# Performance work log

Measured on AMD Instinct MI355X. Metric: run time of the kernel, lower is better.

## Reference

```python
import jax, jax.numpy as jnp
import numpy as np
import math

B, S, H = 1, 2048, 2048
NH, NKV, HD = 32, 8, 64
GROUPS = NH // NKV
WINDOW = 128
ROPE_THETA = 150000.0
FACTOR = 32.0
ORIG_MAX = 4096.0
BETA_FAST = 32.0
BETA_SLOW = 1.0
SCALE = 1.0 / math.sqrt(HD)


def yarn_rope(q, k, position_ids):
    # q: [B,S,NH,HD], k: [B,S,NKV,HD]
    dim_half = HD // 2
    inv_freq = 1.0 / ROPE_THETA ** (jnp.arange(0, dim_half, 2, dtype=jnp.float32) / dim_half)
    wavelengths = 2.0 * jnp.pi / inv_freq
    ratio = ORIG_MAX / wavelengths
    alpha = jnp.clip((FACTOR * ratio - BETA_FAST) / (BETA_SLOW - BETA_FAST), 0.0, 1.0)
    inv_freq_scaled = inv_freq / FACTOR ** alpha
    freqs = position_ids[:, :, None].astype(jnp.float32) * inv_freq_scaled[None, None, :]
    freqs = jnp.repeat(freqs, 2, axis=-1)  # [B,S,dim_half]
    cos = jnp.cos(freqs)[:, :, None, :]
    sin = jnp.sin(freqs)[:, :, None, :]

    def rotate_half(x):
        # Faithful to source: x already has last dim == dim_half, so x2 is empty
        # and rotate_half(x) == x. Kept literal for exactness.
        x1 = x[..., :dim_half]
        x2 = x[..., dim_half:]
        return jnp.concatenate([-x2, x1], axis=-1)

    q_rot = q[..., :dim_half]
    k_rot = k[..., :dim_half]
    q_rot = q_rot * cos + rotate_half(q_rot) * sin
    k_rot = k_rot * cos + rotate_half(k_rot) * sin
    q = jnp.concatenate([q_rot, q[..., dim_half:]], axis=-1)
    k = jnp.concatenate([k_rot, k[..., dim_half:]], axis=-1)
    return q, k


def setup_inputs() -> dict:
    key = jax.random.key(0)
    ks = jax.random.split(key, 5)
    std = 0.02
    hidden_states = jax.random.normal(ks[0], (B, S, H), dtype=jnp.float32)
    position_ids = jnp.broadcast_to(jnp.arange(S, dtype=jnp.int32)[None, :], (B, S))
    Wq = jax.random.normal(ks[1], (H, NH * HD), dtype=jnp.float32) * std
    Wk = jax.random.normal(ks[2], (H, NKV * HD), dtype=jnp.float32) * std
    Wv = jax.random.normal(ks[3], (H, NKV * HD), dtype=jnp.float32) * std
    Wo = jax.random.normal(ks[4], (NH * HD, H), dtype=jnp.float32) * std
    return {"hidden_states": hidden_states, "position_ids": position_ids,
            "Wq": Wq, "Wk": Wk, "Wv": Wv, "Wo": Wo}


def reference(hidden_states, position_ids, Wq, Wk, Wv, Wo):
    q = (hidden_states @ Wq).reshape(B, S, NH, HD)
    k = (hidden_states @ Wk).reshape(B, S, NKV, HD)
    v = (hidden_states @ Wv).reshape(B, S, NKV, HD)
    q, k = yarn_rope(q, k, position_ids)
    # GQA: repeat kv heads to match query heads
    k = jnp.repeat(k, GROUPS, axis=2)  # [B,S,NH,HD]
    v = jnp.repeat(v, GROUPS, axis=2)
    # scores: [B,NH,S,S]
    scores = jnp.einsum('bqhd,bkhd->bhqk', q, k) * SCALE
    row = jnp.arange(S)[:, None]
    col = jnp.arange(S)[None, :]
    mask = ((jnp.abs(row - col) <= WINDOW) & (row >= col)).astype(jnp.float32)
    scores = scores + (1.0 - mask)[None, None, :, :] * -1e9
    attn = jax.nn.softmax(scores, axis=-1)
    out = jnp.einsum('bhqk,bkhd->bqhd', attn, v).reshape(B, S, NH * HD)
    return out @ Wo
```

## Files before the change

kernel.cpp:

```cpp
#include <hip/hip_runtime.h>

typedef unsigned short u16;
typedef short short8 __attribute__((ext_vector_type(8)));
typedef float f32x4 __attribute__((ext_vector_type(4)));

#define SLEN 2048
#define QKV_LD 3072
#define KOFF 2048
#define VOFF 2560

__device__ __forceinline__ u16 f2b(float f){
  unsigned u = __float_as_uint(f);
  u = u + 0x7FFFu + ((u >> 16) & 1u);
  return (u16)(u >> 16);
}
__device__ __forceinline__ float b2f(u16 v){
  unsigned u = ((unsigned)v) << 16;
  return __uint_as_float(u);
}

__device__ __forceinline__ void gload16(const u16* g, u16* l){
  __builtin_amdgcn_global_load_lds((const __attribute__((address_space(1))) void*)g,
                                   (__attribute__((address_space(3))) void*)l, 16, 0, 0);
}

__global__ __launch_bounds__(256) void k_prep(const float* __restrict__ hidden, u16* __restrict__ hb,
                                              const int* __restrict__ pos, float* __restrict__ g,
                                              const float* __restrict__ Wq, const float* __restrict__ Wk,
                                              const float* __restrict__ Wv,
                                              u16* __restrict__ Wcat){
  __shared__ float tile[64][68];
  int b = blockIdx.x, t = threadIdx.x;
  if (b < 4096){
    int i = b * 256 + t;
    float4 v = ((const float4*)hidden)[i];
    ushort4 o;
    o.x = f2b(v.x); o.y = f2b(v.y); o.z = f2b(v.z); o.w = f2b(v.w);
    ((ushort4*)hb)[i] = o;
    return;
  }
  if (b < 4224){
    int idx = (b - 4096) * 256 + t;
    int s = idx >> 4, i = idx & 15;
    float inv = 1.0f / powf(150000.0f, (float)i / 16.0f);
    float wl = 6.283185307179586f / inv;
    float ratio = 4096.0f / wl;
    float alpha = (32.0f * ratio - 32.0f) / (1.0f - 32.0f);
    alpha = fminf(fmaxf(alpha, 0.0f), 1.0f);
    float invs = inv / powf(32.0f, alpha);
    float th = (float)pos[s] * invs;
    double tt = (double)th;
    g[idx] = (float)(cos(tt) + sin(tt));
    return;
  }
  b -= 4224;
  const float* W; int Nw, rowoff;
  if (b < 1024)      { W = Wq; Nw = 2048; rowoff = 0; }
  else if (b < 1280) { W = Wk; Nw = 512;  rowoff = 2048; b -= 1024; }
  else               { W = Wv; Nw = 512;  rowoff = 2560; b -= 1280; }
  const int kt = b & 31, nt = b >> 5;
  const int k0 = kt * 64, n0 = nt * 64;
  #pragma unroll
  for (int i = 0; i < 4; ++i){
    int slot = i * 256 + t;
    int r = slot >> 4, c4 = (slot & 15) * 4;
    float4 v = *(const float4*)&W[(size_t)(k0 + r) * Nw + n0 + c4];
    tile[r][c4] = v.x; tile[r][c4+1] = v.y; tile[r][c4+2] = v.z; tile[r][c4+3] = v.w;
  }
  __syncthreads();
  #pragma unroll
  for (int i = 0; i < 4; ++i){
    int slot = i * 256 + t;
    int nl = slot >> 4, k4 = (slot & 15) * 4;
    ushort4 o;
    o.x = f2b(tile[k4][nl]);   o.y = f2b(tile[k4+1][nl]);
    o.z = f2b(tile[k4+2][nl]); o.w = f2b(tile[k4+3][nl]);
    *(ushort4*)&Wcat[(size_t)(rowoff + n0 + nl) * 2048 + k0 + k4] = o;
  }
}

template<int OUTF32, int ROPE, int BM, int BN, int MINW, int NBUF>
__global__ __launch_bounds__(256, MINW) void k_gemm(const u16* __restrict__ A, const u16* __restrict__ Bt,
                                                    void* __restrict__ C, const float* __restrict__ g,
                                                    int M, int N, int K){
  constexpr int AG = BM / 32;
  constexpr int BG = BN / 32;
  constexpr int ASZ = BM * 64;
  constexpr int BSZ = BN * 64;
  constexpr int MR = BM / 32;
  constexpr int NR = BN / 32;
  __shared__ __align__(16) u16 Smem[NBUF * (ASZ + BSZ)];
  const int tid = threadIdx.x;
  const int lane = tid & 63;
  const int w = tid >> 6;
  const int wr = (w >> 1) * (BM / 2);
  const int wc = (w & 1) * (BN / 2);

  const int nbx = M / BM;
  const int nb  = nbx * (N / BN);
  const int q8  = nb >> 3;
  const int bo  = blockIdx.x;
  const int id2 = (bo & 7) * q8 + (bo >> 3);
  const int m0 = (id2 % nbx) * BM;
  const int n0 = (id2 / nbx) * BN;

  const int rl = lane >> 3;
  const int sc = ((lane & 7) ^ rl) << 3;
  const u16* Ag[AG]; const u16* Bg[BG];
  int Ad[AG], Bd[BG];
  #pragma unroll
  for (int i = 0; i < AG; ++i){
    int row0 = w * (AG * 8) + i * 8;
    Ag[i] = A + (size_t)(m0 + row0 + rl) * K + sc;
    Ad[i] = row0 * 64;
  }
  #pragma unroll
  for (int i = 0; i < BG; ++i){
    int row0 = w * (BG * 8) + i * 8;
    Bg[i] = Bt + (size_t)(n0 + row0 + rl) * K + sc;
    Bd[i] = NBUF * ASZ + row0 * 64;
  }

  const int fr = lane & 15;
  const int g4 = lane >> 4;

  f32x4 acc[MR][NR] = {};

  auto stage = [&](int buf, int k0){
    #pragma unroll
    for (int i = 0; i < AG; ++i) gload16(Ag[i] + k0, Smem + Ad[i] + buf * ASZ);
    #pragma unroll
    for (int i = 0; i < BG; ++i) gload16(Bg[i] + k0, Smem + Bd[i] + buf * BSZ);
  };

  auto compute = [&](int buf){
    const u16* Asb = Smem + buf * ASZ;
    const u16* Bsb = Smem + NBUF * ASZ + buf * BSZ;
    #pragma unroll
    for (int kk = 0; kk < 2; ++kk){
      const int sw = (((kk * 4 + g4)) ^ (fr & 7)) << 3;
      short8 af[MR], bf[NR];
      #pragma unroll
      for (int m = 0; m < MR; ++m)
        af[m] = *(const short8*)&Asb[(wr + m * 16 + fr) * 64 + sw];
      #pragma unroll
      for (int j = 0; j < NR; ++j)
        bf[j] = *(const short8*)&Bsb[(wc + j * 16 + fr) * 64 + sw];
      #pragma unroll
      for (int m = 0; m < MR; ++m)
        #pragma unroll
        for (int j = 0; j < NR; ++j)
          acc[m][j] = __builtin_amdgcn_mfma_f32_16x16x32_bf16(af[m], bf[j], acc[m][j], 0, 0, 0);
    }
  };

  stage(0, 0);
  int buf = 0;
  const int nt = K >> 6;
  if constexpr (NBUF == 2){
    for (int kt = 0; kt < nt; ++kt){
      asm volatile("s_waitcnt vmcnt(0)" ::: "memory");
      __builtin_amdgcn_s_barrier();
      __builtin_amdgcn_sched_barrier(0);
      if (kt + 1 < nt) stage(buf ^ 1, (kt + 1) << 6);
      compute(buf);
      buf ^= 1;
    }
  } else {
    for (int kt = 0; kt < nt; ++kt){
      int nxt = (buf + 1 == NBUF) ? 0 : buf + 1;
      if (kt + 1 < nt){
        stage(nxt, (kt + 1) << 6);
        if constexpr (AG + BG == 6)      asm volatile("s_waitcnt vmcnt(6)" ::: "memory");
        else if constexpr (AG + BG == 7) asm volatile("s_waitcnt vmcnt(7)" ::: "memory");
        else                             asm volatile("s_waitcnt vmcnt(8)" ::: "memory");
      } else {
        asm volatile("s_waitcnt vmcnt(0)" ::: "memory");
      }
      __builtin_amdgcn_s_barrier();
      __builtin_amdgcn_sched_barrier(0);
      compute(buf);
      buf = nxt;
    }
  }

  const int r4 = g4 * 4;
  #pragma unroll
  for (int m = 0; m < MR; ++m)
    #pragma unroll
    for (int j = 0; j < NR; ++j)
      #pragma unroll
      for (int v = 0; v < 4; ++v){
        size_t row = (size_t)(m0 + wr + m * 16 + r4 + v);
        size_t col = (size_t)(n0 + wc + j * 16 + fr);
        float x = acc[m][j][v];
        if (OUTF32){
          ((float*)C)[row * N + col] = x;
        } else {
          if (ROPE){
            int c = (int)col;
            int cj = c & 63;
            if (c < 2560 && cj < 32) x *= g[row * 16 + (cj >> 1)];
            if (c < 2048) x *= 0.18033688f;
          }
          ((u16*)C)[row * N + col] = f2b(x);
        }
      }
}

#define PST 168
__global__ __launch_bounds__(512, 4) void k_attn(const u16* __restrict__ qkv, u16* __restrict__ aout,
                                                 const float* __restrict__ Wo, u16* __restrict__ Wot){
  __shared__ __align__(16) u16 Vt[64 * 264];
  __shared__ __align__(16) u16 P[8 * 16 * PST];
  const int tid = threadIdx.x;
  const int lane = tid & 63;
  const int w = tid >> 6;
  const int id = blockIdx.x;
  const int id2 = (id & 7) * 64 + (id >> 3);
  const int h = id2 >> 4;
  const int q0 = (id2 & 15) * 128;
  const int kvh = h >> 2;
  const int kv0 = q0 - 128;

  {
    const u16* Vg = qkv + VOFF + kvh * 64;
    #pragma unroll
    for (int i = 0; i < 4; ++i){
      int slot = i * 512 + tid;
      int kk = slot >> 3, d8 = (slot & 7) * 8;
      int ks = kv0 + kk; if (ks < 0) ks = 0;
      int ck = kk ^ ((d8 >> 4) << 3);
      short8 v = *(const short8*)(Vg + (size_t)ks * QKV_LD + d8);
      #pragma unroll
      for (int e = 0; e < 8; ++e) Vt[(d8 + e) * 264 + ck] = (u16)v[e];
    }
  }

  const int fr = lane & 15;
  const int kc8 = (lane >> 4) * 8;
  const int r4 = (lane >> 4) * 4;
  const int tt = w >> 2;
  const int wl = w & 3;
  const int nw0 = wl & ~1;
  const int c0 = nw0 * 16;
  const int qt = q0 + tt * 64;
  const int kbase = qt - 128;
  u16* Pw = P + w * 16 * PST;
  const u16* Qg = qkv + h * 64;
  const u16* Kg = qkv + KOFF + kvh * 64;

  short8 qa[2];
  {
    int qrow = qt + wl * 16 + fr;
    qa[0] = *(const short8*)(Qg + (size_t)qrow * QKV_LD + kc8);
    qa[1] = *(const short8*)(Qg + (size_t)qrow * QKV_LD + 32 + kc8);
  }

  f32x4 sc[10];
  __builtin_amdgcn_s_setprio(1);
  #pragma unroll
  for (int n = 0; n < 10; ++n){
    int kr = kbase + (nw0 + n) * 16 + fr;
    int krc = kr < 0 ? 0 : kr;
    short8 kb0 = *(const short8*)(Kg + (size_t)krc * QKV_LD + kc8);
    short8 kb1 = *(const short8*)(Kg + (size_t)krc * QKV_LD + 32 + kc8);
    f32x4 z = {0.f, 0.f, 0.f, 0.f};
    z = __builtin_amdgcn_mfma_f32_16x16x32_bf16(qa[0], kb0, z, 0, 0, 0);
    z = __builtin_amdgcn_mfma_f32_16x16x32_bf16(qa[1], kb1, z, 0, 0, 0);
    sc[n] = z;
  }
  __builtin_amdgcn_s_setprio(0);

  float inv_l[4];
  #pragma unroll
  for (int j = 0; j < 4; ++j){
    int q = qt + wl * 16 + r4 + j;
    float mx = -3.0e38f;
    #pragma unroll
    for (int n = 0; n < 10; ++n){
      int key = kbase + (nw0 + n) * 16 + fr;
      bool valid = (key >= 0) && (key <= q) && (key >= q - 128);
      float s = valid ? sc[n][j] : -1.0e30f;
      sc[n][j] = s;
      mx = fmaxf(mx, s);
    }
    mx = fmaxf(mx, __shfl_xor(mx, 1));
    mx = fmaxf(mx, __shfl_xor(mx, 2));
    mx = fmaxf(mx, __shfl_xor(mx, 4));
    mx = fmaxf(mx, __shfl_xor(mx, 8));
    float sum = 0.f;
    #pragma unroll
    for (int n = 0; n < 10; ++n){
      float pp = exp2f(sc[n][j] - mx);
      sc[n][j] = pp;
      sum += pp;
    }
    sum += __shfl_xor(sum, 1);
    sum += __shfl_xor(sum, 2);
    sum += __shfl_xor(sum, 4);
    sum += __shfl_xor(sum, 8);
    inv_l[j] = 1.0f / sum;
  }

  #pragma unroll
  for (int n = 0; n < 10; ++n)
    #pragma unroll
    for (int j = 0; j < 4; ++j)
      Pw[(r4 + j) * PST + n * 16 + fr] = f2b(sc[n][j]);

  asm volatile("s_waitcnt lgkmcnt(0)" ::: "memory");
  __syncthreads();

  f32x4 ov[4] = {};
  __builtin_amdgcn_s_setprio(1);
  #pragma unroll
  for (int kc = 0; kc < 5; ++kc){
    short8 pa = *(const short8*)&Pw[fr * PST + kc * 32 + kc8];
    #pragma unroll
    for (int f = 0; f < 4; ++f){
      short8 vb = *(const short8*)&Vt[(f * 16 + fr) * 264 + tt * 64 + c0 + kc * 32 + (kc8 ^ (f << 3))];
      ov[f] = __builtin_amdgcn_mfma_f32_16x16x32_bf16(pa, vb, ov[f], 0, 0, 0);
    }
  }
  __builtin_amdgcn_s_setprio(0);

  #pragma unroll
  for (int f = 0; f < 4; ++f)
    #pragma unroll
    for (int j = 0; j < 4; ++j){
      int q = qt + wl * 16 + r4 + j;
      int col = h * 64 + f * 16 + fr;
      aout[(size_t)q * 2048 + col] = f2b(ov[f][j] * inv_l[j]);
    }

  __syncthreads();
  float (*tf)[68] = (float(*)[68])Vt;
  #pragma unroll
  for (int tix = 0; tix < 2; ++tix){
    int tile = id * 2 + tix;
    int kt2 = tile & 31, nt2 = tile >> 5;
    int k0 = kt2 * 64, n0 = nt2 * 64;
    #pragma unroll
    for (int i = 0; i < 2; ++i){
      int slot = i * 512 + tid;
      int r = slot >> 4, c4 = (slot & 15) * 4;
      float4 v = *(const float4*)&Wo[(size_t)(k0 + r) * 2048 + n0 + c4];
      tf[r][c4] = v.x; tf[r][c4+1] = v.y; tf[r][c4+2] = v.z; tf[r][c4+3] = v.w;
    }
    __syncthreads();
    #pragma unroll
    for (int i = 0; i < 2; ++i){
      int slot = i * 512 + tid;
      int nl = slot >> 4, k4 = (slot & 15) * 4;
      ushort4 o;
      o.x = f2b(tf[k4][nl]);   o.y = f2b(tf[k4+1][nl]);
      o.z = f2b(tf[k4+2][nl]); o.w = f2b(tf[k4+3][nl]);
      *(ushort4*)&Wot[(size_t)(n0 + nl) * 2048 + k0 + k4] = o;
    }
    __syncthreads();
  }
}

extern "C" void kernel_launch(void* const* d_in, const int* in_sizes, int n_in,
                              void* d_out, int out_size, void* d_ws, size_t ws_size,
                              hipStream_t stream) {
  const float* hidden = (const float*)d_in[0];
  const int*   pos    = (const int*)d_in[1];
  const float* Wq     = (const float*)d_in[2];
  const float* Wk     = (const float*)d_in[3];
  const float* Wv     = (const float*)d_in[4];
  const float* Wo     = (const float*)d_in[5];
  float* out = (float*)d_out;
  char* ws = (char*)d_ws;

  u16*  hb   = (u16*)(ws);
  u16*  Wcat = (u16*)(ws + ((size_t)8 << 20));
  u16*  Wot  = (u16*)(ws + ((size_t)20 << 20));
  u16*  QKV  = (u16*)(ws + ((size_t)28 << 20));
  float* gtab = (float*)(ws + ((size_t)40 << 20));
  u16*  aout = hb;

  k_prep<<<5760, 256, 0, stream>>>(hidden, hb, pos, gtab, Wq, Wk, Wv, Wcat);
  k_gemm<0,1,128,96,2,2><<<512, 256, 0, stream>>>(hb, Wcat, QKV, gtab, 2048, 3072, 2048);
  k_attn<<<512, 512, 0, stream>>>(QKV, aout, Wo, Wot);
  k_gemm<1,0,64,128,2,3><<<512, 256, 0, stream>>>(aout, Wot, out, nullptr, 2048, 2048, 2048);
}
```

Baseline: 93.10 us.

## Fuse hidden-state bf16 conversion into QKV GEMM A-tile loading

Result: slower. 103.4 us (+11.0%).

```diff
diff --git a/kernel.cpp b/kernel.cpp
--- a/kernel.cpp
+++ b/kernel.cpp
@@ -24,23 +24,14 @@
                                    (__attribute__((address_space(3))) void*)l, 16, 0, 0);
 }
 
-__global__ __launch_bounds__(256) void k_prep(const float* __restrict__ hidden, u16* __restrict__ hb,
-                                              const int* __restrict__ pos, float* __restrict__ g,
+__global__ __launch_bounds__(256) void k_prep(const int* __restrict__ pos, float* __restrict__ g,
                                               const float* __restrict__ Wq, const float* __restrict__ Wk,
                                               const float* __restrict__ Wv,
                                               u16* __restrict__ Wcat){
   __shared__ float tile[64][68];
   int b = blockIdx.x, t = threadIdx.x;
-  if (b < 4096){
-    int i = b * 256 + t;
-    float4 v = ((const float4*)hidden)[i];
-    ushort4 o;
-    o.x = f2b(v.x); o.y = f2b(v.y); o.z = f2b(v.z); o.w = f2b(v.w);
-    ((ushort4*)hb)[i] = o;
-    return;
-  }
-  if (b < 4224){
-    int idx = (b - 4096) * 256 + t;
+  if (b < 128){
+    int idx = b * 256 + t;
     int s = idx >> 4, i = idx & 15;
     float inv = 1.0f / powf(150000.0f, (float)i / 16.0f);
     float wl = 6.283185307179586f / inv;
@@ -53,7 +44,7 @@
     g[idx] = (float)(cos(tt) + sin(tt));
     return;
   }
-  b -= 4224;
+  b -= 128;
   const float* W; int Nw, rowoff;
   if (b < 1024)      { W = Wq; Nw = 2048; rowoff = 0; }
   else if (b < 1280) { W = Wk; Nw = 512;  rowoff = 2048; b -= 1024; }
@@ -79,8 +70,9 @@
   }
 }
 
-template<int OUTF32, int ROPE, int BM, int BN, int MINW, int NBUF>
-__global__ __launch_bounds__(256, MINW) void k_gemm(const u16* __restrict__ A, const u16* __restrict__ Bt,
+template<int OUTF32, int ROPE, int BM, int BN, int MINW, int NBUF, int AF32>
+__global__ __launch_bounds__(256, MINW) void k_gemm(const u16* __restrict__ A, const float* __restrict__ Af,
+                                                    const u16* __restrict__ Bt,
                                                     void* __restrict__ C, const float* __restrict__ g,
                                                     int M, int N, int K){
   constexpr int AG = BM / 32;
@@ -111,7 +103,7 @@
   #pragma unroll
   for (int i = 0; i < AG; ++i){
     int row0 = w * (AG * 8) + i * 8;
-    Ag[i] = A + (size_t)(m0 + row0 + rl) * K + sc;
+    if constexpr (!AF32) Ag[i] = A + (size_t)(m0 + row0 + rl) * K + sc;
     Ad[i] = row0 * 64;
   }
   #pragma unroll
@@ -126,9 +118,7 @@
 
   f32x4 acc[MR][NR] = {};
 
-  auto stage = [&](int buf, int k0){
-    #pragma unroll
-    for (int i = 0; i < AG; ++i) gload16(Ag[i] + k0, Smem + Ad[i] + buf * ASZ);
+  auto stageB = [&](int buf, int k0){
     #pragma unroll
     for (int i = 0; i < BG; ++i) gload16(Bg[i] + k0, Smem + Bd[i] + buf * BSZ);
   };
@@ -154,19 +144,57 @@
     }
   };
 
-  stage(0, 0);
-  int buf = 0;
   const int nt = K >> 6;
-  if constexpr (NBUF == 2){
+  if constexpr (AF32){
+    float4 areg[AG][2];
+    const float* Asrc[AG];
+    #pragma unroll
+    for (int i = 0; i < AG; ++i)
+      Asrc[i] = Af + (size_t)(m0 + w * (AG * 8) + i * 8 + rl) * K + sc;
+    auto loadA = [&](int k0){
+      #pragma unroll
+      for (int i = 0; i < AG; ++i){
+        areg[i][0] = *(const float4*)(Asrc[i] + k0);
+        areg[i][1] = *(const float4*)(Asrc[i] + k0 + 4);
+      }
+    };
+    auto writeA = [&](int buf){
+      #pragma unroll
+      for (int i = 0; i < AG; ++i){
+        short8 o;
+        o[0] = (short)f2b(areg[i][0].x); o[1] = (short)f2b(areg[i][0].y);
+        o[2] = (short)f2b(areg[i][0].z); o[3] = (short)f2b(areg[i][0].w);
+        o[4] = (short)f2b(areg[i][1].x); o[5] = (short)f2b(areg[i][1].y);
+        o[6] = (short)f2b(areg[i][1].z); o[7] = (short)f2b(areg[i][1].w);
+        *(short8*)&Smem[Ad[i] + buf * ASZ + lane * 8] = o;
+      }
+    };
+    stageB(0, 0); loadA(0);
+    asm volatile("s_waitcnt vmcnt(0)" ::: "memory");
+    writeA(0);
+    asm volatile("s_waitcnt lgkmcnt(0)" ::: "memory");
+    __builtin_amdgcn_s_barrier();
+    int buf = 0;
     for (int kt = 0; kt < nt; ++kt){
-      asm volatile("s_waitcnt vmcnt(0)" ::: "memory");
-      __builtin_amdgcn_s_barrier();
       __builtin_amdgcn_sched_barrier(0);
-      if (kt + 1 < nt) stage(buf ^ 1, (kt + 1) << 6);
+      if (kt + 1 < nt){ stageB(buf ^ 1, (kt + 1) << 6); loadA((kt + 1) << 6); }
       compute(buf);
+      if (kt + 1 < nt){
+        asm volatile("s_waitcnt vmcnt(0)" ::: "memory");
+        writeA(buf ^ 1);
+        asm volatile("s_waitcnt lgkmcnt(0)" ::: "memory");
+        __builtin_amdgcn_s_barrier();
+      }
       buf ^= 1;
     }
   } else {
+    auto stage = [&](int buf, int k0){
+      #pragma unroll
+      for (int i = 0; i < AG; ++i) gload16(Ag[i] + k0, Smem + Ad[i] + buf * ASZ);
+      stageB(buf, k0);
+    };
+    stage(0, 0);
+    int buf = 0;
     for (int kt = 0; kt < nt; ++kt){
       int nxt = (buf + 1 == NBUF) ? 0 : buf + 1;
       if (kt + 1 < nt){
@@ -374,15 +402,14 @@
   float* out = (float*)d_out;
   char* ws = (char*)d_ws;
 
-  u16*  hb   = (u16*)(ws);
+  u16*  aout = (u16*)(ws);
   u16*  Wcat = (u16*)(ws + ((size_t)8 << 20));
   u16*  Wot  = (u16*)(ws + ((size_t)20 << 20));
   u16*  QKV  = (u16*)(ws + ((size_t)28 << 20));
   float* gtab = (float*)(ws + ((size_t)40 << 20));
-  u16*  aout = hb;
-
-  k_prep<<<5760, 256, 0, stream>>>(hidden, hb, pos, gtab, Wq, Wk, Wv, Wcat);
-  k_gemm<0,1,128,96,2,2><<<512, 256, 0, stream>>>(hb, Wcat, QKV, gtab, 2048, 3072, 2048);
+
+  k_prep<<<1664, 256, 0, stream>>>(pos, gtab, Wq, Wk, Wv, Wcat);
+  k_gemm<0,1,128,96,2,2,1><<<512, 256, 0, stream>>>(nullptr, hidden, Wcat, QKV, gtab, 2048, 3072, 2048);
   k_attn<<<512, 512, 0, stream>>>(QKV, aout, Wo, Wot);
-  k_gemm<1,0,64,128,2,3><<<512, 256, 0, stream>>>(aout, Wot, out, nullptr, 2048, 2048, 2048);
-}
+  k_gemm<1,0,64,128,2,3,0><<<512, 256, 0, stream>>>(aout, nullptr, Wot, out, nullptr, 2048, 2048, 2048);
+}
```
